# Kernel optimization log

Hardware: AMD Instinct MI355X
Metric: run time of the kernel (lower is better)

## Reference

```python
import jax, jax.numpy as jnp
import numpy as np

D, W, H = 128, 128, 128          # volume obj_shape (d, w, h)
RES_D, RES_H = 180, 180          # detector resolution
SR_D, SR_W, SR_H = 1, 1, 1       # sample rates
BATCH = 4                        # hardcoded batch_size in the torch module


def _trilinear_zeros(vol, cx, cy, cz):
    """torch.grid_sample 5D, mode=trilinear, align_corners=True, padding=zeros.
    vol: [D, W, H]. cx indexes last dim (H), cy indexes W, cz indexes D; all in [-1,1].
    """
    d, w, h = vol.shape
    ix = (cx + 1.0) * 0.5 * (h - 1)
    iy = (cy + 1.0) * 0.5 * (w - 1)
    iz = (cz + 1.0) * 0.5 * (d - 1)
    x0 = jnp.floor(ix); y0 = jnp.floor(iy); z0 = jnp.floor(iz)
    wx1 = ix - x0; wy1 = iy - y0; wz1 = iz - z0
    wx0 = 1.0 - wx1; wy0 = 1.0 - wy1; wz0 = 1.0 - wz1

    def corner(zf, yf, xf, wgt):
        valid = (zf >= 0) & (zf <= d - 1) & (yf >= 0) & (yf <= w - 1) & (xf >= 0) & (xf <= h - 1)
        zi = jnp.clip(zf, 0, d - 1).astype(jnp.int32)
        yi = jnp.clip(yf, 0, w - 1).astype(jnp.int32)
        xi = jnp.clip(xf, 0, h - 1).astype(jnp.int32)
        return jnp.where(valid, vol[zi, yi, xi] * wgt, 0.0)

    return (corner(z0,     y0,     x0,     wz0 * wy0 * wx0)
          + corner(z0,     y0,     x0 + 1, wz0 * wy0 * wx1)
          + corner(z0,     y0 + 1, x0,     wz0 * wy1 * wx0)
          + corner(z0,     y0 + 1, x0 + 1, wz0 * wy1 * wx1)
          + corner(z0 + 1, y0,     x0,     wz1 * wy0 * wx0)
          + corner(z0 + 1, y0,     x0 + 1, wz1 * wy0 * wx1)
          + corner(z0 + 1, y0 + 1, x0,     wz1 * wy1 * wx0)
          + corner(z0 + 1, y0 + 1, x0 + 1, wz1 * wy1 * wx1))


def _project_one(vol, emi_pos, spacing):
    # vol: [D, W, H], emi_pos: [3], spacing: [3]
    K = SR_W * W
    p0y = jnp.linspace(0.0, W - 1.0, K)                     # (P0 - I0)·N, N = [0,1,0]
    lin_x = jnp.linspace(-RES_D / 2.0, RES_D / 2.0 - 1.0, RES_D * SR_D)
    lin_y = jnp.linspace(-RES_H / 2.0, RES_H / 2.0 - 1.0, RES_H * SR_H)
    gx, gy = jnp.meshgrid(lin_x, lin_y, indexing='ij')      # [Nx, Ny]
    I = jnp.stack([gx, jnp.zeros_like(gx), gy], axis=-1) - emi_pos   # [Nx,Ny,3]
    dxv = I / I[..., 1:2]
    dx = jnp.linalg.norm(dxv * spacing, axis=-1)            # per-ray path length [Nx,Ny]
    In = I / jnp.linalg.norm(I, axis=-1, keepdims=True)     # unit ray dirs
    T = (p0y - emi_pos[1])[None, None, :] / In[..., 1:2]    # [Nx,Ny,K]
    grid = In[..., None, :] * T[..., None] + emi_pos        # world points [Nx,Ny,K,3]
    # normalization as in torch code, then torch.flip(grid,[3]) swaps coord order
    cx = grid[..., 2] / H * 2.0          # -> indexes last vol dim (H)
    cy = grid[..., 1] / W * 2.0 - 1.0    # -> indexes W
    cz = grid[..., 0] / D * 2.0          # -> indexes D
    samp = _trilinear_zeros(vol, cx, cy, cz)                # [Nx,Ny,K]
    return jnp.sum(samp, axis=-1) * dx                      # [Nx,Ny]


def setup_inputs() -> dict:
    key = jax.random.key(0)
    k1, k2 = jax.random.split(key)
    I_rec = jax.random.uniform(k1, (1, 1, D, W, H), dtype=jnp.float32)
    # emitters near [0, -300, 0]; y must be far from the y=0 detector plane
    poses = jnp.array([0.0, -300.0, 0.0], jnp.float32) + 5.0 * jax.random.normal(k2, (BATCH, 3), jnp.float32)
    spacing = jnp.ones((3,), jnp.float32)
    return {"I_rec": I_rec, "poses": poses, "spacing": spacing}


def reference(I_rec, poses, spacing):
    vol = I_rec[0, 0]  # [D, W, H]
    # deterministic idx = [0..BATCH-1] (original uses random.sample)
    proj = jax.vmap(_project_one, in_axes=(None, 0, None))(vol, poses[:BATCH], spacing)
    return proj[:, None, :, :]  # [BATCH, 1, RES_D*SR_D, RES_H*SR_H]
```

## Files before the change

kernel.cpp:

```cpp
#include <hip/hip_runtime.h>


#define RES 180
#define NPIX (4 * RES * RES)
#define PPB 32
#define NCHUNK (NPIX / PPB)
#define CHUNK_STRIDE 1013

typedef struct __attribute__((packed, aligned(4))) { float x, y; } f2u;

__global__ __launch_bounds__(256) void proj_kernel(
    const float* __restrict__ vol, const float* __restrict__ poses,
    const float* __restrict__ spacing, float* __restrict__ out) {
  const int tid = threadIdx.x;
  const int lp  = tid & 31;
  const int ks  = tid >> 5;
  const int chunk = (int)(((long long)blockIdx.x * CHUNK_STRIDE) % NCHUNK);
  const int gpix = chunk * PPB + lp;

  const int b   = gpix / (RES * RES);
  const int rem = gpix - b * (RES * RES);
  const int i   = rem / RES;
  const int j   = rem - i * RES;

  const float ex = poses[b * 3 + 0];
  const float ey = poses[b * 3 + 1];
  const float ez = poses[b * 3 + 2];

  const float Ix = ((float)i - 90.0f) - ex;
  const float Iy = -ey;
  const float Iz = ((float)j - 90.0f) - ez;

  const float c     = 63.5f / 64.0f;
  const float invIy = 1.0f / Iy;

  const float izb = fmaf(ex + Ix, c, 63.5f);
  const float izs = Ix * invIy * c;
  const float ixb = fmaf(ez + Iz, c, 63.5f);
  const float ixs = Iz * invIy * c;

  float ka = 0.0f, kb = 128.0f;
  if (ixs > 1e-12f)       { ka = fmaxf(ka, (-1.0f - ixb) / ixs); kb = fminf(kb, (128.0f - ixb) / ixs); }
  else if (ixs < -1e-12f) { ka = fmaxf(ka, (128.0f - ixb) / ixs); kb = fminf(kb, (-1.0f - ixb) / ixs); }
  else if (ixb <= -1.0f || ixb >= 128.0f) { kb = ka; }
  if (izs > 1e-12f)       { ka = fmaxf(ka, (-1.0f - izb) / izs); kb = fminf(kb, (128.0f - izb) / izs); }
  else if (izs < -1e-12f) { ka = fmaxf(ka, (128.0f - izb) / izs); kb = fminf(kb, (-1.0f - izb) / izs); }
  else if (izb <= -1.0f || izb >= 128.0f) { kb = ka; }
  ka = fmaxf(ka, 0.0f);
  kb = fminf(kb, 128.0f);
  const int kai = (int)ceilf(ka);
  const int kbi = (int)ceilf(kb);

  const int c1 = ks;
  const int c2 = 15 - ks;
  const int a1 = max(kai, 8 * c1), b1 = min(kbi, 8 * c1 + 8);
  const int a2 = max(kai, 8 * c2), b2 = min(kbi, 8 * c2 + 8);
  const int n1 = max(0, b1 - a1);
  const int n2 = max(0, b2 - a2);
  const int nt = max(n1, n2);

  float sum = 0.0f;

#define BODY(kk)                                                               \
  {                                                                            \
    const int k = (kk);                                                        \
    const float kf = (float)k;                                                 \
    const float ix = fmaf(kf, ixs, ixb);                                       \
    const float iy = kf * c;                                                   \
    const float iz = fmaf(kf, izs, izb);                                       \
    const float fx = floorf(ix), fy = floorf(iy), fz = floorf(iz);             \
    const int x0 = (int)fx, y0 = (int)fy, z0 = (int)fz;                        \
    const float wx1 = ix - fx, wy1 = iy - fy, wz1 = iz - fz;                   \
    const float wx0 = 1.0f - wx1, wy0 = 1.0f - wy1, wz0 = 1.0f - wz1;          \
    const float vx0 = ((unsigned)x0       < 128u) ? wx0 : 0.0f;                \
    const float vx1 = ((unsigned)(x0 + 1) < 128u) ? wx1 : 0.0f;                \
    const float vz0 = ((unsigned)z0       < 128u) ? wz0 : 0.0f;                \
    const float vz1 = ((unsigned)(z0 + 1) < 128u) ? wz1 : 0.0f;                \
    const int xb2 = min(max(x0, 0), 126);                                      \
    const bool inx = (x0 == xb2);                                              \
    const float wlo = inx ? vx0 : vx1;                                         \
    const float whi = inx ? vx1 : vx0;                                         \
    const int zc0 = min(max(z0, 0), 127), zc1 = min(max(z0 + 1, 0), 127);      \
    const float* base = vol + ((zc0 << 14) + (y0 << 7) + xb2);                 \
    const int dz = (zc1 - zc0) << 14;                                          \
    const f2u v00 = *(const f2u*)(base);                                       \
    const f2u v01 = *(const f2u*)(base + 128);                                 \
    const f2u v10 = *(const f2u*)(base + dz);                                  \
    const f2u v11 = *(const f2u*)(base + dz + 128);                            \
    const float s00 = fmaf(whi, v00.y, wlo * v00.x);                           \
    const float s01 = fmaf(whi, v01.y, wlo * v01.x);                           \
    const float s10 = fmaf(whi, v10.y, wlo * v10.x);                           \
    const float s11 = fmaf(whi, v11.y, wlo * v11.x);                           \
    const float s0  = fmaf(wy1, s01, wy0 * s00);                               \
    const float s1  = fmaf(wy1, s11, wy0 * s10);                               \
    sum = fmaf(vz0, s0, sum);                                                  \
    sum = fmaf(vz1, s1, sum);                                                  \
  }

  for (int t = 0; t < nt; ++t) {
    if (t < n1) BODY(a1 + t)
    if (t < n2) BODY(a2 + t)
  }
#undef BODY

  __shared__ float part[256];
  part[tid] = sum;
  __syncthreads();

  if (tid < PPB) {
    float tot = 0.0f;
#pragma unroll
    for (int s = 0; s < 8; ++s) tot += part[tid + 32 * s];
    const float ax = Ix * invIy * spacing[0];
    const float az = Iz * invIy * spacing[2];
    const float sy = spacing[1];
    out[gpix] = tot * sqrtf(fmaf(ax, ax, fmaf(az, az, sy * sy)));
  }
}

extern "C" void kernel_launch(void* const* d_in, const int* in_sizes, int n_in,
                              void* d_out, int out_size, void* d_ws, size_t ws_size,
                              hipStream_t stream) {
  const float* vol     = (const float*)d_in[0];
  const float* poses   = (const float*)d_in[1];
  const float* spacing = (const float*)d_in[2];
  float* out = (float*)d_out;

  proj_kernel<<<NCHUNK, 256, 0, stream>>>(vol, poses, spacing, out);
}
```

Before: 25.92 us.

## Split ray samples into contiguous per-warp ranges with unmasked interior loop

Each of the 8 warps in a block now takes a contiguous 16-sample slice of the ray instead of two interleaved 8-sample chunks. Within that slice it computes the sub-range where all trilinear corners are in bounds, and runs a fast loop there with no clamping or validity masks. A masked prologue and epilogue handle the boundary samples. This cuts per-sample ALU work, but the old balancing of chunks from opposite ends of the ray is lost, so warps can do uneven amounts of work. The float-derived interior bounds also rely on the endpoint checks to avoid out-of-bounds reads.

```diff
diff --git a/kernel.cpp b/kernel.cpp
--- a/kernel.cpp
+++ b/kernel.cpp
@@ -39,32 +39,46 @@
   const float ixb = fmaf(ez + Iz, c, 63.5f);
   const float ixs = Iz * invIy * c;
 
-  float ka = 0.0f, kb = 128.0f;
+  const int k0 = ks * 16;
+  float ka = (float)k0, kb = (float)(k0 + 16);
   if (ixs > 1e-12f)       { ka = fmaxf(ka, (-1.0f - ixb) / ixs); kb = fminf(kb, (128.0f - ixb) / ixs); }
   else if (ixs < -1e-12f) { ka = fmaxf(ka, (128.0f - ixb) / ixs); kb = fminf(kb, (-1.0f - ixb) / ixs); }
   else if (ixb <= -1.0f || ixb >= 128.0f) { kb = ka; }
   if (izs > 1e-12f)       { ka = fmaxf(ka, (-1.0f - izb) / izs); kb = fminf(kb, (128.0f - izb) / izs); }
   else if (izs < -1e-12f) { ka = fmaxf(ka, (128.0f - izb) / izs); kb = fminf(kb, (-1.0f - izb) / izs); }
   else if (izb <= -1.0f || izb >= 128.0f) { kb = ka; }
-  ka = fmaxf(ka, 0.0f);
-  kb = fminf(kb, 128.0f);
+  ka = fmaxf(ka, (float)k0);
+  kb = fminf(kb, (float)(k0 + 16));
   const int kai = (int)ceilf(ka);
   const int kbi = (int)ceilf(kb);
 
-  const int c1 = ks;
-  const int c2 = 15 - ks;
-  const int a1 = max(kai, 8 * c1), b1 = min(kbi, 8 * c1 + 8);
-  const int a2 = max(kai, 8 * c2), b2 = min(kbi, 8 * c2 + 8);
-  const int n1 = max(0, b1 - a1);
-  const int n2 = max(0, b2 - a2);
-  const int nt = max(n1, n2);
+  float la = ka, lb = kb;
+  if (ixs > 1e-12f)       { la = fmaxf(la, (0.0f - ixb) / ixs); lb = fminf(lb, (127.0f - ixb) / ixs); }
+  else if (ixs < -1e-12f) { la = fmaxf(la, (127.0f - ixb) / ixs); lb = fminf(lb, (0.0f - ixb) / ixs); }
+  else if (ixb < 0.0f || ixb >= 127.0f) { lb = la; }
+  if (izs > 1e-12f)       { la = fmaxf(la, (0.0f - izb) / izs); lb = fminf(lb, (127.0f - izb) / izs); }
+  else if (izs < -1e-12f) { la = fmaxf(la, (127.0f - izb) / izs); lb = fminf(lb, (0.0f - izb) / izs); }
+  else if (izb < 0.0f || izb >= 127.0f) { lb = la; }
+  int l0 = (int)ceilf(la);
+  int l1 = (int)ceilf(lb);
+  l0 = min(max(l0, kai), kbi);
+  l1 = min(max(l1, l0), kbi);
+  if (l1 > l0) {
+    const float x_ = fmaf((float)l0, ixs, ixb), z_ = fmaf((float)l0, izs, izb);
+    if (!(x_ >= 0.0f && x_ < 127.0f && z_ >= 0.0f && z_ < 127.0f)) ++l0;
+  }
+  if (l1 > l0) {
+    const float x_ = fmaf((float)(l1 - 1), ixs, ixb), z_ = fmaf((float)(l1 - 1), izs, izb);
+    if (!(x_ >= 0.0f && x_ < 127.0f && z_ >= 0.0f && z_ < 127.0f)) --l1;
+  }
+  if (l1 < l0) l1 = l0;
 
   float sum = 0.0f;
 
-#define BODY(kk)                                                               \
+#define MASKED_BODY(kk)                                                        \
   {                                                                            \
-    const int k = (kk);                                                        \
-    const float kf = (float)k;                                                 \
+    const int mk = (kk);                                                       \
+    const float kf = (float)mk;                                                \
     const float ix = fmaf(kf, ixs, ixb);                                       \
     const float iy = kf * c;                                                   \
     const float iz = fmaf(kf, izs, izb);                                       \
@@ -97,11 +111,37 @@
     sum = fmaf(vz1, s1, sum);                                                  \
   }
 
-  for (int t = 0; t < nt; ++t) {
-    if (t < n1) BODY(a1 + t)
-    if (t < n2) BODY(a2 + t)
+  for (int k = kai; k < l0; ++k) MASKED_BODY(k)
+
+#pragma unroll 2
+  for (int k = l0; k < l1; ++k) {
+    const float kf = (float)k;
+    const float ix = fmaf(kf, ixs, ixb);
+    const float iy = kf * c;
+    const float iz = fmaf(kf, izs, izb);
+    const float fx = floorf(ix), fy = floorf(iy), fz = floorf(iz);
+    const int x0 = (int)fx, y0 = (int)fy, z0 = (int)fz;
+    const float wx1 = ix - fx, wy1 = iy - fy, wz1 = iz - fz;
+    const float wx0 = 1.0f - wx1, wy0 = 1.0f - wy1, wz0 = 1.0f - wz1;
+
+    const float* base = vol + ((z0 << 14) + (y0 << 7) + x0);
+    const f2u v00 = *(const f2u*)(base);
+    const f2u v01 = *(const f2u*)(base + 128);
+    const f2u v10 = *(const f2u*)(base + 16384);
+    const f2u v11 = *(const f2u*)(base + 16384 + 128);
+
+    const float s00 = fmaf(wx1, v00.y, wx0 * v00.x);
+    const float s01 = fmaf(wx1, v01.y, wx0 * v01.x);
+    const float s10 = fmaf(wx1, v10.y, wx0 * v10.x);
+    const float s11 = fmaf(wx1, v11.y, wx0 * v11.x);
+    const float s0  = fmaf(wy1, s01, wy0 * s00);
+    const float s1  = fmaf(wy1, s11, wy0 * s10);
+    sum = fmaf(wz0, s0, sum);
+    sum = fmaf(wz1, s1, sum);
   }
-#undef BODY
+
+  for (int k = l1; k < kbi; ++k) MASKED_BODY(k)
+#undef MASKED_BODY
 
   __shared__ float part[256];
   part[tid] = sum;
```

After: 32.05 us. +23.7%, slower.
